# Kernel tuning notes

Measured on AMD Instinct MI355X. Metric: run time of the kernel, lower is better.

The kernel has to match this reference:

```python
import jax, jax.numpy as jnp
import numpy as np

N_NODES = 100000
K = 5
C = 16
E = 3200000  # nonzeros per shift power


def setup_inputs() -> dict:
    key = jax.random.key(0)
    k1, k2, k3, k4, k5 = jax.random.split(key, 5)
    X = jax.random.normal(k1, (N_NODES, C), dtype=jnp.float32)
    rows = jax.random.randint(k2, (K, E), 0, N_NODES, dtype=jnp.int32)
    cols = jax.random.randint(k3, (K, E), 0, N_NODES, dtype=jnp.int32)
    vals = jax.random.normal(k4, (K, E), dtype=jnp.float32)
    h = jax.random.normal(k5, (C, K), dtype=jnp.float32)  # per-channel filter taps
    return {"X": X, "rows": rows, "cols": cols, "vals": vals, "h": h}


def reference(X, rows, cols, vals, h):
    # Original math: y = sum_c sum_k h[c,k] * (S_k @ X[:, c])
    #              = sum_k S_k @ (X @ h[:, k])
    N = X.shape[0]
    Kp, Ep = rows.shape
    Z = X @ h  # [N, K] combined per-tap signals
    # gather Z at source nodes for each tap: Zg[k, e] = Z[cols[k, e], k]
    Zg = Z[cols, jnp.arange(Kp, dtype=cols.dtype)[:, None]]  # [K, E]
    contrib = vals * Zg  # [K, E]
    y = jax.ops.segment_sum(contrib.reshape(-1), rows.reshape(-1), num_segments=N)
    return y  # [N]
```

## Files before the change

kernel.cpp:

```cpp
#include <hip/hip_runtime.h>
#include <hip/hip_fp16.h>

#define N_NODES 100000
#define KK 5
#define CC 16
#define EE 3200000
#define NXCC 8

#define NB 16
#define ROWS_PB 6250
#define WCAP 512
#define WPAD 513
#define BPB 64
#define CHUNK 5120
#define NCHUNK 3125
#define BLK_PER_K 625

typedef unsigned int uint2v __attribute__((ext_vector_type(2)));

__device__ __forceinline__ int xcc_id() {
    int x;
    asm volatile("s_getreg_b32 %0, hwreg(HW_REG_XCC_ID)" : "=s"(x));
    return x & (NXCC - 1);
}

__device__ __forceinline__ float ldg_l2(const float* p) {
    return __hip_atomic_load(p, __ATOMIC_RELAXED, __HIP_MEMORY_SCOPE_AGENT);
}

__global__ void compute_z_kernel(const float* __restrict__ X,
                                 const float* __restrict__ h,
                                 float* __restrict__ Zt) {
    int n = blockIdx.x * blockDim.x + threadIdx.x;
    if (n >= N_NODES) return;
    const float4* Xr = (const float4*)(X + (size_t)n * CC);
    float4 x0 = Xr[0], x1 = Xr[1], x2 = Xr[2], x3 = Xr[3];
    float xv[CC] = {x0.x, x0.y, x0.z, x0.w, x1.x, x1.y, x1.z, x1.w,
                    x2.x, x2.y, x2.z, x2.w, x3.x, x3.y, x3.z, x3.w};
#pragma unroll
    for (int k = 0; k < KK; ++k) {
        float acc = 0.0f;
#pragma unroll
        for (int c = 0; c < CC; ++c) acc += xv[c] * h[c * KK + k];
        Zt[k * N_NODES + n] = acc;
    }
}

__global__ __launch_bounds__(512, 2)
void scatter_kernel(const int* __restrict__ rows,
                    const int* __restrict__ cols,
                    const float* __restrict__ vals,
                    const float* __restrict__ Zt,
                    unsigned int* __restrict__ binned,
                    int* __restrict__ counts,
                    float* __restrict__ spill) {
    __shared__ int lcnt[NB];
    __shared__ unsigned int buf[NB * WPAD];
    int tid = threadIdx.x;
    if (tid < NB) lcnt[tid] = 0;
    __syncthreads();

    int w = blockIdx.x;
    int cbase = w * CHUNK;
    const float* Zk = Zt + (size_t)(w / BLK_PER_K) * N_NODES;

    int e0 = cbase + tid * 4;
    int e1 = cbase + 2048 + tid * 4;
    int e2 = cbase + 4096 + tid * 2;
    int4   r0 = *(const int4*)(rows + e0);
    int4   c0 = *(const int4*)(cols + e0);
    float4 v0 = *(const float4*)(vals + e0);
    int4   r1 = *(const int4*)(rows + e1);
    int4   c1 = *(const int4*)(cols + e1);
    float4 v1 = *(const float4*)(vals + e1);
    int2   r2 = *(const int2*)(rows + e2);
    int2   c2 = *(const int2*)(cols + e2);
    float2 v2 = *(const float2*)(vals + e2);

    float z[10];
    z[0] = ldg_l2(&Zk[c0.x]); z[1] = ldg_l2(&Zk[c0.y]);
    z[2] = ldg_l2(&Zk[c0.z]); z[3] = ldg_l2(&Zk[c0.w]);
    z[4] = ldg_l2(&Zk[c1.x]); z[5] = ldg_l2(&Zk[c1.y]);
    z[6] = ldg_l2(&Zk[c1.z]); z[7] = ldg_l2(&Zk[c1.w]);
    z[8] = ldg_l2(&Zk[c2.x]); z[9] = ldg_l2(&Zk[c2.y]);

    int   rr[10] = {r0.x, r0.y, r0.z, r0.w, r1.x, r1.y, r1.z, r1.w, r2.x, r2.y};
    float vv[10] = {v0.x, v0.y, v0.z, v0.w, v1.x, v1.y, v1.z, v1.w, v2.x, v2.y};

    int pos[10];
#pragma unroll
    for (int i = 0; i < 10; ++i) {
        int b = rr[i] / ROWS_PB;
        pos[i] = atomicAdd(&lcnt[b], 1);
    }

#pragma unroll
    for (int i = 0; i < 10; ++i) {
        int b = rr[i] / ROWS_PB;
        float cb = vv[i] * z[i];
        int p = pos[i];
        if (p < WCAP) {
            unsigned int packed =
                ((unsigned)(rr[i] - b * ROWS_PB) << 16) |
                (unsigned)__half_as_ushort(__float2half_rn(cb));
            buf[b * WPAD + p] = packed;
        } else {
            unsafeAtomicAdd(&spill[rr[i]], cb);
        }
    }
    __syncthreads();

    unsigned int* wbase = binned + (size_t)w * WCAP;
#pragma unroll 1
    for (int b = 0; b < NB; ++b) {
        int cnt = min(lcnt[b], WCAP);
        unsigned int* dst = wbase + (size_t)b * ((size_t)NCHUNK * WCAP);
        if (tid < cnt) dst[tid] = buf[b * WPAD + tid];
    }
    if (tid < NB) counts[w * NB + tid] = min(lcnt[tid], WCAP);
}

__global__ __launch_bounds__(512, 2)
void accum_kernel(const unsigned int* __restrict__ binned,
                  const int* __restrict__ counts,
                  float* __restrict__ partials) {
    __shared__ float acc[ROWS_PB];
    __shared__ int cnts[56];
    int b = blockIdx.x / BPB;
    int s = blockIdx.x % BPB;
    int tid = threadIdx.x;
    int wlo = (NCHUNK * s) / BPB;
    int whi = (NCHUNK * (s + 1)) / BPB;
    for (int i = tid; i < ROWS_PB; i += 512) acc[i] = 0.0f;
    if (tid < whi - wlo) cnts[tid] = counts[(wlo + tid) * NB + b];
    __syncthreads();

    const unsigned int* bbase = binned + (size_t)b * ((size_t)NCHUNK * WCAP);
    int t    = tid & 255;
    int half = tid >> 8;
    for (int w0 = wlo; w0 < whi; w0 += 16) {
        uint2v e[8];
        int ok0[8], ok1[8];
#pragma unroll
        for (int j = 0; j < 8; ++j) {
            int w = w0 + 2 * j + half;
            int cnt = (w < whi) ? cnts[w - wlo] : 0;
            ok0[j] = 2 * t < cnt;
            ok1[j] = 2 * t + 1 < cnt;
            const uint2v* src = (const uint2v*)(bbase + (size_t)w * WCAP);
            uint2v ez = {0u, 0u};
            e[j] = ok0[j] ? src[t] : ez;
        }
#pragma unroll
        for (int j = 0; j < 8; ++j) {
            if (ok0[j])
                atomicAdd(&acc[e[j][0] >> 16],
                          __half2float(__ushort_as_half((unsigned short)(e[j][0] & 0xFFFFu))));
            if (ok1[j])
                atomicAdd(&acc[e[j][1] >> 16],
                          __half2float(__ushort_as_half((unsigned short)(e[j][1] & 0xFFFFu))));
        }
    }
    __syncthreads();
    float* dst = partials + (size_t)blockIdx.x * ROWS_PB;
    for (int i = tid; i < ROWS_PB; i += 512) dst[i] = acc[i];
}

__global__ void reduce_kernel(const float* __restrict__ partials,
                              const float* __restrict__ spill,
                              float* __restrict__ y) {
    int n = blockIdx.x * blockDim.x + threadIdx.x;
    if (n >= N_NODES) return;
    int b = n / ROWS_PB, loc = n - b * ROWS_PB;
    const float* p = partials + (size_t)(b * BPB) * ROWS_PB + loc;
    float acc = spill[n];
#pragma unroll 8
    for (int s = 0; s < BPB; ++s) acc += p[(size_t)s * ROWS_PB];
    y[n] = acc;
}

__global__ void edge_kernel_atomic(const int* __restrict__ rows,
                                   const int* __restrict__ cols,
                                   const float* __restrict__ vals,
                                   const float* __restrict__ Zt,
                                   float* __restrict__ yrep) {
    int t = blockIdx.x * blockDim.x + threadIdx.x;
    int base = t * 4;
    if (base >= KK * EE) return;
    int k = base / EE;
    const float* Zk = Zt + (size_t)k * N_NODES;
    float* y = yrep + (size_t)xcc_id() * N_NODES;
    int4 r = *(const int4*)(rows + base);
    int4 c = *(const int4*)(cols + base);
    float4 v = *(const float4*)(vals + base);
    unsafeAtomicAdd(&y[r.x], v.x * Zk[c.x]);
    unsafeAtomicAdd(&y[r.y], v.y * Zk[c.y]);
    unsafeAtomicAdd(&y[r.z], v.z * Zk[c.z]);
    unsafeAtomicAdd(&y[r.w], v.w * Zk[c.w]);
}

__global__ void reduce8_kernel(const float* __restrict__ yrep, float* __restrict__ y) {
    int n = blockIdx.x * blockDim.x + threadIdx.x;
    if (n >= N_NODES) return;
    float acc = 0.0f;
#pragma unroll
    for (int r = 0; r < NXCC; ++r) acc += yrep[(size_t)r * N_NODES + n];
    y[n] = acc;
}

extern "C" void kernel_launch(void* const* d_in, const int* in_sizes, int n_in,
                              void* d_out, int out_size, void* d_ws, size_t ws_size,
                              hipStream_t stream) {
    const float* X    = (const float*)d_in[0];
    const int*   rows = (const int*)  d_in[1];
    const int*   cols = (const int*)  d_in[2];
    const float* vals = (const float*)d_in[3];
    const float* h    = (const float*)d_in[4];
    float* y = (float*)d_out;

    char* ws = (char*)d_ws;
    float* Zt = (float*)ws;
    size_t counts_off  = 2000000;
    size_t spill_off   = counts_off + 200000;
    size_t binned_off  = spill_off + 400000;
    size_t binned_sz   = (size_t)NCHUNK * NB * WCAP * 4;
    size_t partial_off = binned_off + binned_sz;
    size_t partial_sz  = (size_t)NB * BPB * ROWS_PB * 4;
    size_t need = partial_off + partial_sz;

    {
        int threads = 256;
        int blocks  = (N_NODES + threads - 1) / threads;
        compute_z_kernel<<<blocks, threads, 0, stream>>>(X, h, Zt);
    }

    if (ws_size >= need) {
        int*          counts   = (int*)(ws + counts_off);
        float*        spill    = (float*)(ws + spill_off);
        unsigned int* binned   = (unsigned int*)(ws + binned_off);
        float*        partials = (float*)(ws + partial_off);
        hipMemsetAsync(spill, 0, 400000, stream);
        scatter_kernel<<<NCHUNK, 512, 0, stream>>>(rows, cols, vals, Zt,
                                                   binned, counts, spill);
        accum_kernel<<<NB * BPB, 512, 0, stream>>>(binned, counts, partials);
        {
            int threads = 256;
            int blocks  = (N_NODES + threads - 1) / threads;
            reduce_kernel<<<blocks, threads, 0, stream>>>(partials, spill, y);
        }
    } else {
        float* yrep = (float*)(ws + spill_off);
        hipMemsetAsync(yrep, 0, (size_t)NXCC * N_NODES * sizeof(float), stream);
        {
            int threads = 256;
            int blocks = ((KK * EE) / 4 + threads - 1) / threads;
            edge_kernel_atomic<<<blocks, threads, 0, stream>>>(rows, cols, vals, Zt, yrep);
        }
        {
            int threads = 256;
            int blocks  = (N_NODES + threads - 1) / threads;
            reduce8_kernel<<<blocks, threads, 0, stream>>>(yrep, y);
        }
    }
}
```

Baseline: 358.3 us.

## Make scatter persistent, stage fp16 Z slice in LDS, shrink bin capacity

The scatter kernel becomes persistent: 256 blocks each loop over a contiguous range of chunks. When the tap index changes, each block stages up to 64K entries of an fp16 copy of Z into LDS, and gathers hit LDS for low column indices while the rest fall back to global fp16. The per-bin capacity drops from 512 to 384, which reduces binned memory traffic but sends more entries to the atomic spill path. Staging is chosen at runtime through occupancy queries, and the fp16 Z adds rounding error on top of the existing fp16 packing.

```diff
diff --git a/kernel.cpp b/kernel.cpp
--- a/kernel.cpp
+++ b/kernel.cpp
@@ -9,12 +9,13 @@
 
 #define NB 16
 #define ROWS_PB 6250
-#define WCAP 512
-#define WPAD 513
+#define WCAP 384
+#define WPAD 385
 #define BPB 64
 #define CHUNK 5120
 #define NCHUNK 3125
 #define BLK_PER_K 625
+#define SGRID 256
 
 typedef unsigned int uint2v __attribute__((ext_vector_type(2)));
 
@@ -24,13 +25,10 @@
     return x & (NXCC - 1);
 }
 
-__device__ __forceinline__ float ldg_l2(const float* p) {
-    return __hip_atomic_load(p, __ATOMIC_RELAXED, __HIP_MEMORY_SCOPE_AGENT);
-}
-
 __global__ void compute_z_kernel(const float* __restrict__ X,
                                  const float* __restrict__ h,
-                                 float* __restrict__ Zt) {
+                                 float* __restrict__ Zt,
+                                 __half* __restrict__ Zh) {
     int n = blockIdx.x * blockDim.x + threadIdx.x;
     if (n >= N_NODES) return;
     const float4* Xr = (const float4*)(X + (size_t)n * CC);
@@ -43,81 +41,106 @@
 #pragma unroll
         for (int c = 0; c < CC; ++c) acc += xv[c] * h[c * KK + k];
         Zt[k * N_NODES + n] = acc;
-    }
-}
-
+        Zh[k * N_NODES + n] = __float2half_rn(acc);
+    }
+}
+
+template<int SN>
 __global__ __launch_bounds__(512, 2)
-void scatter_kernel(const int* __restrict__ rows,
-                    const int* __restrict__ cols,
-                    const float* __restrict__ vals,
-                    const float* __restrict__ Zt,
-                    unsigned int* __restrict__ binned,
-                    int* __restrict__ counts,
-                    float* __restrict__ spill) {
+void scatter_lds_kernel(const int* __restrict__ rows,
+                        const int* __restrict__ cols,
+                        const float* __restrict__ vals,
+                        const __half* __restrict__ Zh,
+                        unsigned int* __restrict__ binned,
+                        int* __restrict__ counts,
+                        float* __restrict__ spill) {
+    extern __shared__ char dynlds[];
+    __half*       zsl = (__half*)dynlds;
+    unsigned int* buf = (unsigned int*)(dynlds + (size_t)SN * 2);
     __shared__ int lcnt[NB];
-    __shared__ unsigned int buf[NB * WPAD];
     int tid = threadIdx.x;
-    if (tid < NB) lcnt[tid] = 0;
-    __syncthreads();
-
-    int w = blockIdx.x;
-    int cbase = w * CHUNK;
-    const float* Zk = Zt + (size_t)(w / BLK_PER_K) * N_NODES;
-
-    int e0 = cbase + tid * 4;
-    int e1 = cbase + 2048 + tid * 4;
-    int e2 = cbase + 4096 + tid * 2;
-    int4   r0 = *(const int4*)(rows + e0);
-    int4   c0 = *(const int4*)(cols + e0);
-    float4 v0 = *(const float4*)(vals + e0);
-    int4   r1 = *(const int4*)(rows + e1);
-    int4   c1 = *(const int4*)(cols + e1);
-    float4 v1 = *(const float4*)(vals + e1);
-    int2   r2 = *(const int2*)(rows + e2);
-    int2   c2 = *(const int2*)(cols + e2);
-    float2 v2 = *(const float2*)(vals + e2);
-
-    float z[10];
-    z[0] = ldg_l2(&Zk[c0.x]); z[1] = ldg_l2(&Zk[c0.y]);
-    z[2] = ldg_l2(&Zk[c0.z]); z[3] = ldg_l2(&Zk[c0.w]);
-    z[4] = ldg_l2(&Zk[c1.x]); z[5] = ldg_l2(&Zk[c1.y]);
-    z[6] = ldg_l2(&Zk[c1.z]); z[7] = ldg_l2(&Zk[c1.w]);
-    z[8] = ldg_l2(&Zk[c2.x]); z[9] = ldg_l2(&Zk[c2.y]);
-
-    int   rr[10] = {r0.x, r0.y, r0.z, r0.w, r1.x, r1.y, r1.z, r1.w, r2.x, r2.y};
-    float vv[10] = {v0.x, v0.y, v0.z, v0.w, v1.x, v1.y, v1.z, v1.w, v2.x, v2.y};
-
-    int pos[10];
-#pragma unroll
-    for (int i = 0; i < 10; ++i) {
-        int b = rr[i] / ROWS_PB;
-        pos[i] = atomicAdd(&lcnt[b], 1);
-    }
-
-#pragma unroll
-    for (int i = 0; i < 10; ++i) {
-        int b = rr[i] / ROWS_PB;
-        float cb = vv[i] * z[i];
-        int p = pos[i];
-        if (p < WCAP) {
-            unsigned int packed =
-                ((unsigned)(rr[i] - b * ROWS_PB) << 16) |
-                (unsigned)__half_as_ushort(__float2half_rn(cb));
-            buf[b * WPAD + p] = packed;
-        } else {
-            unsafeAtomicAdd(&spill[rr[i]], cb);
-        }
-    }
-    __syncthreads();
-
-    unsigned int* wbase = binned + (size_t)w * WCAP;
+    int bid = blockIdx.x;
+    int w0 = (int)(((long long)NCHUNK * bid) / SGRID);
+    int w1 = (int)(((long long)NCHUNK * (bid + 1)) / SGRID);
+
+    int klast = -1;
+    for (int w = w0; w < w1; ++w) {
+        int k = w / BLK_PER_K;
+        const __half* Zk_h = Zh + (size_t)k * N_NODES;
+        if (SN > 0 && k != klast) {
+            __syncthreads();
+            const float4* zsrc = (const float4*)Zk_h;
+            float4*       zdst = (float4*)dynlds;
+#pragma unroll
+            for (int i = 0; i < SN / 4096; ++i)
+                zdst[tid + i * 512] = zsrc[tid + i * 512];
+            klast = k;
+            __syncthreads();
+        }
+        if (tid < NB) lcnt[tid] = 0;
+        __syncthreads();
+
+        int cbase = w * CHUNK;
+        int e0 = cbase + tid * 4;
+        int e1 = cbase + 2048 + tid * 4;
+        int e2 = cbase + 4096 + tid * 2;
+        int4   r0 = *(const int4*)(rows + e0);
+        int4   c0 = *(const int4*)(cols + e0);
+        float4 v0 = *(const float4*)(vals + e0);
+        int4   r1 = *(const int4*)(rows + e1);
+        int4   c1 = *(const int4*)(cols + e1);
+        float4 v1 = *(const float4*)(vals + e1);
+        int2   r2 = *(const int2*)(rows + e2);
+        int2   c2 = *(const int2*)(cols + e2);
+        float2 v2 = *(const float2*)(vals + e2);
+
+        int   cc[10] = {c0.x, c0.y, c0.z, c0.w, c1.x, c1.y, c1.z, c1.w, c2.x, c2.y};
+        int   rr[10] = {r0.x, r0.y, r0.z, r0.w, r1.x, r1.y, r1.z, r1.w, r2.x, r2.y};
+        float vv[10] = {v0.x, v0.y, v0.z, v0.w, v1.x, v1.y, v1.z, v1.w, v2.x, v2.y};
+
+        float z[10];
+#pragma unroll
+        for (int i = 0; i < 10; ++i) {
+            unsigned c = (unsigned)cc[i];
+            __half hz;
+            if (SN > 0 && c < (unsigned)SN) hz = zsl[c];
+            else                            hz = Zk_h[c];
+            z[i] = __half2float(hz);
+        }
+
+        int pos[10];
+#pragma unroll
+        for (int i = 0; i < 10; ++i) {
+            int b = rr[i] / ROWS_PB;
+            pos[i] = atomicAdd(&lcnt[b], 1);
+        }
+
+#pragma unroll
+        for (int i = 0; i < 10; ++i) {
+            int b = rr[i] / ROWS_PB;
+            float cb = vv[i] * z[i];
+            int p = pos[i];
+            if (p < WCAP) {
+                unsigned int packed =
+                    ((unsigned)(rr[i] - b * ROWS_PB) << 16) |
+                    (unsigned)__half_as_ushort(__float2half_rn(cb));
+                buf[b * WPAD + p] = packed;
+            } else {
+                unsafeAtomicAdd(&spill[rr[i]], cb);
+            }
+        }
+        __syncthreads();
+
+        unsigned int* wbase = binned + (size_t)w * WCAP;
 #pragma unroll 1
-    for (int b = 0; b < NB; ++b) {
-        int cnt = min(lcnt[b], WCAP);
-        unsigned int* dst = wbase + (size_t)b * ((size_t)NCHUNK * WCAP);
-        if (tid < cnt) dst[tid] = buf[b * WPAD + tid];
-    }
-    if (tid < NB) counts[w * NB + tid] = min(lcnt[tid], WCAP);
+        for (int b = 0; b < NB; ++b) {
+            int cnt = min(lcnt[b], WCAP);
+            if (tid < cnt)
+                wbase[(size_t)b * ((size_t)NCHUNK * WCAP) + tid] = buf[b * WPAD + tid];
+        }
+        if (tid < NB) counts[w * NB + tid] = min(lcnt[tid], WCAP);
+        __syncthreads();
+    }
 }
 
 __global__ __launch_bounds__(512, 2)
@@ -219,19 +242,21 @@
     float* y = (float*)d_out;
 
     char* ws = (char*)d_ws;
-    float* Zt = (float*)ws;
-    size_t counts_off  = 2000000;
-    size_t spill_off   = counts_off + 200000;
-    size_t binned_off  = spill_off + 400000;
+    float*  Zt = (float*)ws;
+    size_t zh_off      = 2000000;
+    size_t counts_off  = 3000000;
+    size_t spill_off   = 3200000;
+    size_t binned_off  = 3600000;
     size_t binned_sz   = (size_t)NCHUNK * NB * WCAP * 4;
     size_t partial_off = binned_off + binned_sz;
     size_t partial_sz  = (size_t)NB * BPB * ROWS_PB * 4;
     size_t need = partial_off + partial_sz;
+    __half* Zh = (__half*)(ws + zh_off);
 
     {
         int threads = 256;
         int blocks  = (N_NODES + threads - 1) / threads;
-        compute_z_kernel<<<blocks, threads, 0, stream>>>(X, h, Zt);
+        compute_z_kernel<<<blocks, threads, 0, stream>>>(X, h, Zt, Zh);
     }
 
     if (ws_size >= need) {
@@ -240,8 +265,57 @@
         unsigned int* binned   = (unsigned int*)(ws + binned_off);
         float*        partials = (float*)(ws + partial_off);
         hipMemsetAsync(spill, 0, 400000, stream);
-        scatter_kernel<<<NCHUNK, 512, 0, stream>>>(rows, cols, vals, Zt,
-                                                   binned, counts, spill);
+
+        static int g_sn = -1;
+        const size_t stag = (size_t)NB * WPAD * 4;
+        if (g_sn < 0) {
+            g_sn = 0;
+            int nb = 0;
+            hipFuncSetAttribute((const void*)scatter_lds_kernel<65536>,
+                                hipFuncAttributeMaxDynamicSharedMemorySize,
+                                (int)(65536 * 2 + stag));
+            if (hipOccupancyMaxActiveBlocksPerMultiprocessor(
+                    &nb, scatter_lds_kernel<65536>, 512, 65536 * 2 + stag) == hipSuccess
+                && nb >= 1) g_sn = 65536;
+            if (g_sn == 0) {
+                nb = 0;
+                hipFuncSetAttribute((const void*)scatter_lds_kernel<49152>,
+                                    hipFuncAttributeMaxDynamicSharedMemorySize,
+                                    (int)(49152 * 2 + stag));
+                if (hipOccupancyMaxActiveBlocksPerMultiprocessor(
+                        &nb, scatter_lds_kernel<49152>, 512, 49152 * 2 + stag) == hipSuccess
+                    && nb >= 1) g_sn = 49152;
+            }
+            if (g_sn == 0) {
+                nb = 0;
+                hipFuncSetAttribute((const void*)scatter_lds_kernel<32768>,
+                                    hipFuncAttributeMaxDynamicSharedMemorySize,
+                                    (int)(32768 * 2 + stag));
+                if (hipOccupancyMaxActiveBlocksPerMultiprocessor(
+                        &nb, scatter_lds_kernel<32768>, 512, 32768 * 2 + stag) == hipSuccess
+                    && nb >= 1) g_sn = 32768;
+            }
+        }
+        size_t dyn = (size_t)g_sn * 2 + stag;
+        switch (g_sn) {
+        case 65536:
+            scatter_lds_kernel<65536><<<SGRID, 512, dyn, stream>>>(
+                rows, cols, vals, Zh, binned, counts, spill);
+            break;
+        case 49152:
+            scatter_lds_kernel<49152><<<SGRID, 512, dyn, stream>>>(
+                rows, cols, vals, Zh, binned, counts, spill);
+            break;
+        case 32768:
+            scatter_lds_kernel<32768><<<SGRID, 512, dyn, stream>>>(
+                rows, cols, vals, Zh, binned, counts, spill);
+            break;
+        default:
+            scatter_lds_kernel<0><<<SGRID, 512, dyn, stream>>>(
+                rows, cols, vals, Zh, binned, counts, spill);
+            break;
+        }
+
         accum_kernel<<<NB * BPB, 512, 0, stream>>>(binned, counts, partials);
         {
             int threads = 256;
```

Measured after the change: 346.5 us. 3.3% less time.
